# Kernel tuning notes

Measured on AMD Instinct MI355X. Metric: run time of the kernel, lower is better.

The kernel has to match this reference:

```python
import jax, jax.numpy as jnp
import numpy as np

N_NODES = 100000
N_EDGES = 3200000
D_IN = 128
D_OUT = 128

def setup_inputs() -> dict:
    key = jax.random.key(0)
    k1, k2, k3, k4, k5 = jax.random.split(key, 5)
    nodes = jnp.arange(N_NODES, dtype=jnp.int64 if jax.config.jax_enable_x64 else jnp.int32)
    features = jax.random.normal(k1, (N_NODES, D_IN), dtype=jnp.float32)
    edge_index = jax.random.randint(k2, (2, N_EDGES), 0, N_NODES)
    # torch nn.Linear(2*D_IN, D_OUT) params, stored as [in, out]
    bound = 1.0 / np.sqrt(2 * D_IN)
    W = jax.random.uniform(k3, (2 * D_IN, D_OUT), minval=-bound, maxval=bound, dtype=jnp.float32)
    b = jax.random.uniform(k4, (D_OUT,), minval=-bound, maxval=bound, dtype=jnp.float32)
    return {"nodes": nodes, "features": features, "edge_index": edge_index, "W": W, "b": b}

def reference(nodes, features, edge_index, W, b):
    # Mean aggregation over full neighbor lists. gcn=False: edges are treated
    # as undirected (neighbors appended for both src and dst), and output is
    # relu(Linear(concat([self_feats, neigh_feats]))).
    N, d = features.shape
    src, dst = edge_index[0], edge_index[1]
    neigh_sum = (jnp.zeros((N, d), features.dtype)
                 .at[src].add(features[dst])
                 .at[dst].add(features[src]))
    cnt = (jnp.zeros((N,), features.dtype)
           .at[src].add(1.0)
           .at[dst].add(1.0))
    neigh_mean = neigh_sum / jnp.maximum(cnt, 1.0)[:, None]
    combined = jnp.concatenate([features[nodes], neigh_mean[nodes]], axis=1)  # [B, 2d]
    return jax.nn.relu(combined @ W + b)
```

## Files before the change

### kernel.cpp

```cpp
#include <hip/hip_runtime.h>
#include <hip/hip_bf16.h>
#include <cmath>

#define D 128
#define MAXNB 1024
#define TEDGE 2048

typedef __attribute__((ext_vector_type(8))) short bf16x8;
typedef __attribute__((ext_vector_type(4))) float f32x4;

__device__ __forceinline__ unsigned short f2bf(float f) {
    union { __hip_bfloat16 h; unsigned short u; } c;
    c.h = __float2bfloat16(f);
    return c.u;
}

__device__ __forceinline__ void accum8(float* a, uint4 u) {
    a[0] += __uint_as_float(u.x << 16);
    a[1] += __uint_as_float(u.x & 0xffff0000u);
    a[2] += __uint_as_float(u.y << 16);
    a[3] += __uint_as_float(u.y & 0xffff0000u);
    a[4] += __uint_as_float(u.z << 16);
    a[5] += __uint_as_float(u.z & 0xffff0000u);
    a[6] += __uint_as_float(u.w << 16);
    a[7] += __uint_as_float(u.w & 0xffff0000u);
}

__device__ __forceinline__ void accum8f8(float* a, uint2 u) {
    a[0] += __builtin_amdgcn_cvt_f32_fp8((int)u.x, 0);
    a[1] += __builtin_amdgcn_cvt_f32_fp8((int)u.x, 1);
    a[2] += __builtin_amdgcn_cvt_f32_fp8((int)u.x, 2);
    a[3] += __builtin_amdgcn_cvt_f32_fp8((int)u.x, 3);
    a[4] += __builtin_amdgcn_cvt_f32_fp8((int)u.y, 0);
    a[5] += __builtin_amdgcn_cvt_f32_fp8((int)u.y, 1);
    a[6] += __builtin_amdgcn_cvt_f32_fp8((int)u.y, 2);
    a[7] += __builtin_amdgcn_cvt_f32_fp8((int)u.y, 3);
}

__global__ __launch_bounds__(256) void partition_edges(
    const int* __restrict__ ei, int* __restrict__ cursor,
    int* __restrict__ arena, int pbcap, int E, int nb) {
    __shared__ int cnt[MAXNB];
    __shared__ int off[MAXNB + 1];
    __shared__ int gb[MAXNB];
    __shared__ int sb[256];
    __shared__ int stage[2 * TEDGE];
    const int t = threadIdx.x;
    const int e0 = blockIdx.x * TEDGE;
    const int eE = min(e0 + TEDGE, E);

#pragma unroll
    for (int k = 0; k < 4; ++k) cnt[t * 4 + k] = 0;
    __syncthreads();

    int s[8], d[8];
    bool v[8];
#pragma unroll
    for (int q = 0; q < 8; ++q) {
        int e = e0 + t + q * 256;
        v[q] = e < eE;
        if (v[q]) { s[q] = ei[e]; d[q] = ei[E + e]; }
    }

#pragma unroll
    for (int q = 0; q < 8; ++q) if (v[q]) {
        atomicAdd(&cnt[s[q] >> 7], 1);
        atomicAdd(&cnt[d[q] >> 7], 1);
    }
    __syncthreads();

    int c0 = cnt[t * 4], c1 = cnt[t * 4 + 1], c2 = cnt[t * 4 + 2], c3 = cnt[t * 4 + 3];
    sb[t] = c0 + c1 + c2 + c3;
    __syncthreads();
    for (int o = 1; o < 256; o <<= 1) {
        int x = (t >= o) ? sb[t - o] : 0;
        __syncthreads();
        sb[t] += x;
        __syncthreads();
    }
    int run = (t > 0) ? sb[t - 1] : 0;
    off[t * 4] = run; run += c0;
    off[t * 4 + 1] = run; run += c1;
    off[t * 4 + 2] = run; run += c2;
    off[t * 4 + 3] = run;
    if (t == 255) off[MAXNB] = sb[255];

    for (int j = t; j < nb; j += 256) {
        int c = cnt[j];
        gb[j] = c ? atomicAdd(&cursor[j], c) : 0;
    }
    __syncthreads();

#pragma unroll
    for (int k = 0; k < 4; ++k) cnt[t * 4 + k] = off[t * 4 + k];
    __syncthreads();

#pragma unroll
    for (int q = 0; q < 8; ++q) if (v[q]) {
        int ps = atomicAdd(&cnt[s[q] >> 7], 1);
        stage[ps] = ((s[q] & 127) << 17) | d[q];
        int pd = atomicAdd(&cnt[d[q] >> 7], 1);
        stage[pd] = ((d[q] & 127) << 17) | s[q];
    }
    __syncthreads();

    const int total = 2 * (eE - e0);
    for (int p = t; p < total; p += 256) {
        int vv = stage[p];
        int lo = 0, hi = MAXNB;
        while (hi - lo > 1) {
            int mid = (lo + hi) >> 1;
            if (off[mid] <= p) lo = mid; else hi = mid;
        }
        int idx = gb[lo] + (p - off[lo]);
        if (idx < pbcap) arena[(size_t)lo * pbcap + idx] = vv;
    }
}

__global__ __launch_bounds__(256) void bucket_scatter(
    const int* __restrict__ cursor, const int* __restrict__ arena, int pbcap,
    int* __restrict__ deg, int* __restrict__ colp, int cap, int N, int nb) {
    __shared__ int ldeg[128];
    const int t = threadIdx.x;
    for (int b = blockIdx.x; b < nb; b += gridDim.x) {
        if (t < 128) ldeg[t] = 0;
        __syncthreads();
        int cnt = cursor[b];
        if (cnt > pbcap) cnt = pbcap;
        const int* s = arena + (size_t)b * pbcap;
        const size_t cb = (size_t)(b << 7) * cap;
        int i = t;
        for (; i + 768 < cnt; i += 1024) {
            int v0 = s[i], v1 = s[i + 256], v2 = s[i + 512], v3 = s[i + 768];
            int r0 = atomicAdd(&ldeg[v0 >> 17], 1);
            int r1 = atomicAdd(&ldeg[v1 >> 17], 1);
            int r2 = atomicAdd(&ldeg[v2 >> 17], 1);
            int r3 = atomicAdd(&ldeg[v3 >> 17], 1);
            if (r0 < cap) colp[cb + (size_t)(v0 >> 17) * cap + r0] = v0 & 0x1FFFF;
            if (r1 < cap) colp[cb + (size_t)(v1 >> 17) * cap + r1] = v1 & 0x1FFFF;
            if (r2 < cap) colp[cb + (size_t)(v2 >> 17) * cap + r2] = v2 & 0x1FFFF;
            if (r3 < cap) colp[cb + (size_t)(v3 >> 17) * cap + r3] = v3 & 0x1FFFF;
        }
        for (; i < cnt; i += 256) {
            int v = s[i];
            int r = atomicAdd(&ldeg[v >> 17], 1);
            if (r < cap) colp[cb + (size_t)(v >> 17) * cap + r] = v & 0x1FFFF;
        }
        __syncthreads();
        if (t < 128) {
            int node = (b << 7) + t;
            if (node < N) deg[node] = ldeg[t];
        }
        __syncthreads();
    }
}

__global__ __launch_bounds__(256) void bucket_fill(
    const int* __restrict__ ei, int* __restrict__ deg,
    int* __restrict__ colp, int cap, int E) {
    int tid = blockIdx.x * blockDim.x + threadIdx.x;
    int stride = gridDim.x * blockDim.x;
    int e[8], s[8], d[8];
    bool v[8];
#pragma unroll
    for (int q = 0; q < 8; ++q) {
        e[q] = tid + q * stride;
        v[q] = e[q] < E;
    }
#pragma unroll
    for (int q = 0; q < 8; ++q) if (v[q]) { s[q] = ei[e[q]]; d[q] = ei[E + e[q]]; }
    int rs[8], rd[8];
#pragma unroll
    for (int q = 0; q < 8; ++q) if (v[q]) rs[q] = atomicAdd(&deg[s[q]], 1);
#pragma unroll
    for (int q = 0; q < 8; ++q) if (v[q]) rd[q] = atomicAdd(&deg[d[q]], 1);
#pragma unroll
    for (int q = 0; q < 8; ++q) if (v[q] && rs[q] < cap) colp[(size_t)s[q] * cap + rs[q]] = d[q];
#pragma unroll
    for (int q = 0; q < 8; ++q) if (v[q] && rd[q] < cap) colp[(size_t)d[q] * cap + rd[q]] = s[q];
}

__global__ __launch_bounds__(256) void convert_fp8(
    const float4* __restrict__ f, uint2* __restrict__ o, int n8) {
    int i = blockIdx.x * blockDim.x + threadIdx.x;
    int stride = gridDim.x * blockDim.x;
    for (; i < n8; i += stride) {
        float4 a = f[2 * i];
        float4 c = f[2 * i + 1];
        int w0 = __builtin_amdgcn_cvt_pk_fp8_f32(a.x, a.y, 0, false);
        w0 = __builtin_amdgcn_cvt_pk_fp8_f32(a.z, a.w, w0, true);
        int w1 = __builtin_amdgcn_cvt_pk_fp8_f32(c.x, c.y, 0, false);
        w1 = __builtin_amdgcn_cvt_pk_fp8_f32(c.z, c.w, w1, true);
        uint2 r;
        r.x = (unsigned)w0;
        r.y = (unsigned)w1;
        o[i] = r;
    }
}

__global__ __launch_bounds__(256) void convert_bf16(
    const float4* __restrict__ f, uint2* __restrict__ o, int n4) {
    int i = blockIdx.x * blockDim.x + threadIdx.x;
    int stride = gridDim.x * blockDim.x;
    for (; i < n4; i += stride) {
        float4 v = f[i];
        uint2 r;
        r.x = (unsigned)f2bf(v.x) | ((unsigned)f2bf(v.y) << 16);
        r.y = (unsigned)f2bf(v.z) | ((unsigned)f2bf(v.w) << 16);
        o[i] = r;
    }
}

__global__ __launch_bounds__(256) void prepack_w(
    const float* __restrict__ W, unsigned* __restrict__ wb) {
    int id = blockIdx.x * 256 + threadIdx.x;
    if (id >= 4096) return;
    int j = id & 127, ks = id >> 7;
    unsigned hi[4], lo[4];
#pragma unroll
    for (int e = 0; e < 4; ++e) {
        float w0 = W[(size_t)(ks * 8 + 2 * e) * 128 + j];
        float w1 = W[(size_t)(ks * 8 + 2 * e + 1) * 128 + j];
        unsigned short h0 = f2bf(w0), h1 = f2bf(w1);
        float l0f = w0 - __uint_as_float((unsigned)h0 << 16);
        float l1f = w1 - __uint_as_float((unsigned)h1 << 16);
        hi[e] = (unsigned)h0 | ((unsigned)h1 << 16);
        lo[e] = (unsigned)f2bf(l0f) | ((unsigned)f2bf(l1f) << 16);
    }
    ((uint4*)wb)[ks * 128 + j] = make_uint4(hi[0], hi[1], hi[2], hi[3]);
    ((uint4*)wb)[4096 + ks * 128 + j] = make_uint4(lo[0], lo[1], lo[2], lo[3]);
}

__global__ __launch_bounds__(256) void gather_gemm_pad(
    const int* __restrict__ nodes, const float* __restrict__ feat,
    const uint2* __restrict__ fb2,
    const int* __restrict__ deg, const int* __restrict__ colp, int cap,
    const uint4* __restrict__ wb4, const float* __restrict__ b,
    float* __restrict__ out, int B) {
    __shared__ uint4 combQ[512];
    unsigned char* combB = (unsigned char*)combQ;
    const int t = threadIdx.x;
    const int lane = t & 63;
    const int w = t >> 6;
    const int g = lane >> 4;
    const int sub = lane & 15;
    const int base = blockIdx.x * 16;

    {
        int r = t >> 4, sb = t & 15;
        int row = base + r;
        uint4 u = make_uint4(0u, 0u, 0u, 0u);
        if (row < B) {
            const float* fp = feat + (size_t)nodes[row] * D + sb * 8;
            float4 a = *(const float4*)fp;
            float4 c = *(const float4*)(fp + 4);
            u.x = (unsigned)f2bf(a.x) | ((unsigned)f2bf(a.y) << 16);
            u.y = (unsigned)f2bf(a.z) | ((unsigned)f2bf(a.w) << 16);
            u.z = (unsigned)f2bf(c.x) | ((unsigned)f2bf(c.y) << 16);
            u.w = (unsigned)f2bf(c.z) | ((unsigned)f2bf(c.w) << 16);
        }
        int off = (r * 512 + sb * 16) ^ ((r & 7) << 4);
        *(uint4*)(combB + off) = u;
    }

    for (int rq = 0; rq < 4; ++rq) {
        const int rl = w + 4 * rq;
        const int row = base + rl;
        if (row < B) {
            const int node = __builtin_amdgcn_readfirstlane(nodes[row]);
            int degn = deg[node];
            if (degn > cap) degn = cap;
            const int p0 = node * cap;
            float accA[8] = {0, 0, 0, 0, 0, 0, 0, 0};
            float accB[8] = {0, 0, 0, 0, 0, 0, 0, 0};
            int i = 0;
            for (; i + 15 < degn; i += 16) {
                int n0 = colp[p0 + i + g];
                int n1 = colp[p0 + i + 4 + g];
                int n2 = colp[p0 + i + 8 + g];
                int n3 = colp[p0 + i + 12 + g];
                uint2 u0 = fb2[(size_t)n0 * 16 + sub];
                uint2 u1 = fb2[(size_t)n1 * 16 + sub];
                uint2 u2 = fb2[(size_t)n2 * 16 + sub];
                uint2 u3 = fb2[(size_t)n3 * 16 + sub];
                accum8f8(accA, u0);
                accum8f8(accB, u1);
                accum8f8(accA, u2);
                accum8f8(accB, u3);
            }
            for (; i + 7 < degn; i += 8) {
                int n0 = colp[p0 + i + g];
                int n1 = colp[p0 + i + 4 + g];
                uint2 u0 = fb2[(size_t)n0 * 16 + sub];
                uint2 u1 = fb2[(size_t)n1 * 16 + sub];
                accum8f8(accA, u0);
                accum8f8(accB, u1);
            }
            for (; i + 3 < degn; i += 4) {
                int n0 = colp[p0 + i + g];
                accum8f8(accA, fb2[(size_t)n0 * 16 + sub]);
            }
            int rem = degn - i;
            if (g < rem) {
                int n0 = colp[p0 + i + g];
                accum8f8(accB, fb2[(size_t)n0 * 16 + sub]);
            }
            const float inv = (degn > 0) ? 1.0f / (float)degn : 0.0f;
            float vals[8];
#pragma unroll
            for (int k = 0; k < 8; ++k) {
                float v = accA[k] + accB[k];
                v += __shfl_xor(v, 16, 64);
                v += __shfl_xor(v, 32, 64);
                vals[k] = v * inv;
            }
            if (g == 0) {
                unsigned p0u = (unsigned)f2bf(vals[0]) | ((unsigned)f2bf(vals[1]) << 16);
                unsigned p1u = (unsigned)f2bf(vals[2]) | ((unsigned)f2bf(vals[3]) << 16);
                unsigned p2u = (unsigned)f2bf(vals[4]) | ((unsigned)f2bf(vals[5]) << 16);
                unsigned p3u = (unsigned)f2bf(vals[6]) | ((unsigned)f2bf(vals[7]) << 16);
                int off = (rl * 512 + 256 + sub * 16) ^ ((rl & 7) << 4);
                *(uint4*)(combB + off) = make_uint4(p0u, p1u, p2u, p3u);
            }
        } else if (g == 0) {
            int off = (rl * 512 + 256 + sub * 16) ^ ((rl & 7) << 4);
            *(uint4*)(combB + off) = make_uint4(0u, 0u, 0u, 0u);
        }
    }
    __syncthreads();

    const int jl = lane & 15;
    const int kg = lane >> 4;
    const int j0 = w * 32 + jl, j1 = j0 + 16;
    f32x4 acc0 = {0.f, 0.f, 0.f, 0.f};
    f32x4 acc1 = {0.f, 0.f, 0.f, 0.f};
#pragma unroll
    for (int s = 0; s < 8; ++s) {
        int aoff = (jl * 512 + s * 64 + kg * 16) ^ ((jl & 7) << 4);
        bf16x8 a = *(const bf16x8*)(combB + aoff);
        int bi = (s * 4 + kg) * 128;
        bf16x8 bh0 = *(const bf16x8*)&wb4[bi + j0];
        bf16x8 bh1 = *(const bf16x8*)&wb4[bi + j1];
        bf16x8 bl0 = *(const bf16x8*)&wb4[4096 + bi + j0];
        bf16x8 bl1 = *(const bf16x8*)&wb4[4096 + bi + j1];
        acc0 = __builtin_amdgcn_mfma_f32_16x16x32_bf16(a, bh0, acc0, 0, 0, 0);
        acc1 = __builtin_amdgcn_mfma_f32_16x16x32_bf16(a, bh1, acc1, 0, 0, 0);
        acc0 = __builtin_amdgcn_mfma_f32_16x16x32_bf16(a, bl0, acc0, 0, 0, 0);
        acc1 = __builtin_amdgcn_mfma_f32_16x16x32_bf16(a, bl1, acc1, 0, 0, 0);
    }
    const float b0 = b[j0], b1 = b[j1];
    const int r0 = kg * 4;
#pragma unroll
    for (int rg = 0; rg < 4; ++rg) {
        int row = base + r0 + rg;
        if (row < B) {
            out[(size_t)row * D + j0] = fmaxf(acc0[rg] + b0, 0.0f);
            out[(size_t)row * D + j1] = fmaxf(acc1[rg] + b1, 0.0f);
        }
    }
}


__global__ __launch_bounds__(256) void deg_rank(
    const int* __restrict__ ei, int* __restrict__ deg,
    unsigned* __restrict__ rank, int E) {
    int tid = blockIdx.x * blockDim.x + threadIdx.x;
    int stride = gridDim.x * blockDim.x;
    int e[8], s[8], d[8];
    bool v[8];
#pragma unroll
    for (int q = 0; q < 8; ++q) {
        e[q] = tid + q * stride;
        v[q] = e[q] < E;
    }
#pragma unroll
    for (int q = 0; q < 8; ++q) if (v[q]) { s[q] = ei[e[q]]; d[q] = ei[E + e[q]]; }
    int rs[8], rd[8];
#pragma unroll
    for (int q = 0; q < 8; ++q) if (v[q]) rs[q] = atomicAdd(&deg[s[q]], 1);
#pragma unroll
    for (int q = 0; q < 8; ++q) if (v[q]) rd[q] = atomicAdd(&deg[d[q]], 1);
#pragma unroll
    for (int q = 0; q < 8; ++q)
        if (v[q]) rank[e[q]] = (unsigned)rs[q] | ((unsigned)rd[q] << 16);
}

__global__ __launch_bounds__(256) void scan_block(
    const int* __restrict__ deg, int* __restrict__ rowptr,
    int* __restrict__ bsum, int N) {
    __shared__ int lds[256];
    const int t = threadIdx.x;
    const int base = blockIdx.x * 1024 + t * 4;
    int v[4];
#pragma unroll
    for (int k = 0; k < 4; ++k) v[k] = (base + k < N) ? deg[base + k] : 0;
    lds[t] = v[0] + v[1] + v[2] + v[3];
    __syncthreads();
    for (int off = 1; off < 256; off <<= 1) {
        int x = (t >= off) ? lds[t - off] : 0;
        __syncthreads();
        lds[t] += x;
        __syncthreads();
    }
    if (t == 255) bsum[blockIdx.x] = lds[255];
    int run = (t > 0) ? lds[t - 1] : 0;
#pragma unroll
    for (int k = 0; k < 4; ++k) {
        if (base + k < N) rowptr[base + k] = run;
        run += v[k];
    }
}

__global__ __launch_bounds__(1024) void scan_aux(int* __restrict__ bsum, int nb) {
    __shared__ int lds[1024];
    const int t = threadIdx.x;
    int v = (t < nb) ? bsum[t] : 0;
    lds[t] = v;
    __syncthreads();
    for (int off = 1; off < 1024; off <<= 1) {
        int x = (t >= off) ? lds[t - off] : 0;
        __syncthreads();
        lds[t] += x;
        __syncthreads();
    }
    if (t < nb) bsum[t] = lds[t] - v;
}

__global__ __launch_bounds__(256) void scan_finalize(
    int* __restrict__ rowptr, const int* __restrict__ bsum, int N, int twoE) {
    int i = blockIdx.x * blockDim.x + threadIdx.x;
    if (i == 0) rowptr[N] = twoE;
    if (i >= N) return;
    rowptr[i] += bsum[i >> 10];
}

__global__ __launch_bounds__(256) void csr_fill2(
    const int* __restrict__ ei, const int* __restrict__ rowptr,
    const unsigned* __restrict__ rank, int* __restrict__ col, int E) {
    int tid = blockIdx.x * blockDim.x + threadIdx.x;
    int stride = gridDim.x * blockDim.x;
    int e[8], s[8], d[8], ps[8], pd[8];
    unsigned r[8];
    bool v[8];
#pragma unroll
    for (int q = 0; q < 8; ++q) {
        e[q] = tid + q * stride;
        v[q] = e[q] < E;
    }
#pragma unroll
    for (int q = 0; q < 8; ++q) if (v[q]) { s[q] = ei[e[q]]; d[q] = ei[E + e[q]]; r[q] = rank[e[q]]; }
#pragma unroll
    for (int q = 0; q < 8; ++q) if (v[q]) { ps[q] = rowptr[s[q]]; pd[q] = rowptr[d[q]]; }
#pragma unroll
    for (int q = 0; q < 8; ++q) if (v[q]) {
        col[ps[q] + (int)(r[q] & 0xffffu)] = d[q];
        col[pd[q] + (int)(r[q] >> 16)] = s[q];
    }
}

__global__ __launch_bounds__(256) void gather_gemm(
    const int* __restrict__ nodes, const uint4* __restrict__ fb4,
    const int* __restrict__ rowptr, const int* __restrict__ col,
    const float* __restrict__ W, const float* __restrict__ b,
    float* __restrict__ out, int B) {
    __shared__ float comb[16][256];
    const int t = threadIdx.x;
    const int lane = t & 63;
    const int w = t >> 6;
    const int g = lane >> 4;
    const int sub = lane & 15;
    const int base = blockIdx.x * 16;
    {
        int r = t >> 4, sb = t & 15;
        int row = base + r;
        float a[8] = {0, 0, 0, 0, 0, 0, 0, 0};
        if (row < B) accum8(a, fb4[(size_t)nodes[row] * 16 + sb]);
        *(float4*)&comb[r][sb * 8] = make_float4(a[0], a[1], a[2], a[3]);
        *(float4*)&comb[r][sb * 8 + 4] = make_float4(a[4], a[5], a[6], a[7]);
    }
    for (int rq = 0; rq < 4; ++rq) {
        const int rl = w + 4 * rq;
        const int row = base + rl;
        if (row < B) {
            const int node = __builtin_amdgcn_readfirstlane(nodes[row]);
            const int p0 = rowptr[node], p1 = rowptr[node + 1];
            float accA[8] = {0, 0, 0, 0, 0, 0, 0, 0};
            float accB[8] = {0, 0, 0, 0, 0, 0, 0, 0};
            int i = p0;
            for (; i + 7 < p1; i += 8) {
                int na = col[i + g];
                int nb = col[i + 4 + g];
                uint4 ua = fb4[(size_t)na * 16 + sub];
                uint4 ub = fb4[(size_t)nb * 16 + sub];
                accum8(accA, ua);
                accum8(accB, ub);
            }
            for (; i + 3 < p1; i += 4) {
                int na = col[i + g];
                accum8(accA, fb4[(size_t)na * 16 + sub]);
            }
            int rem = p1 - i;
            if (g < rem) {
                int na = col[i + g];
                accum8(accB, fb4[(size_t)na * 16 + sub]);
            }
            const int degn = p1 - p0;
            const float inv = (degn > 0) ? 1.0f / (float)degn : 0.0f;
            float vals[8];
#pragma unroll
            for (int k = 0; k < 8; ++k) {
                float v = accA[k] + accB[k];
                v += __shfl_xor(v, 16, 64);
                v += __shfl_xor(v, 32, 64);
                vals[k] = v * inv;
            }
            if (g == 0) {
                *(float4*)&comb[rl][128 + sub * 8] =
                    make_float4(vals[0], vals[1], vals[2], vals[3]);
                *(float4*)&comb[rl][128 + sub * 8 + 4] =
                    make_float4(vals[4], vals[5], vals[6], vals[7]);
            }
        } else if (g == 0) {
            float4 z = make_float4(0.f, 0.f, 0.f, 0.f);
            *(float4*)&comb[rl][128 + sub * 8] = z;
            *(float4*)&comb[rl][128 + sub * 8 + 4] = z;
        }
    }
    __syncthreads();
    const int j = t & 127;
    const int rr = t >> 7;
    float acc[8];
    const float bj = b[j];
#pragma unroll
    for (int r = 0; r < 8; ++r) acc[r] = bj;
    for (int k4 = 0; k4 < 64; ++k4) {
        float w0 = W[(size_t)(4 * k4 + 0) * 128 + j];
        float w1 = W[(size_t)(4 * k4 + 1) * 128 + j];
        float w2 = W[(size_t)(4 * k4 + 2) * 128 + j];
        float w3 = W[(size_t)(4 * k4 + 3) * 128 + j];
#pragma unroll
        for (int r = 0; r < 8; ++r) {
            float4 c = *(const float4*)&comb[2 * r + rr][4 * k4];
            acc[r] = fmaf(c.x, w0, acc[r]);
            acc[r] = fmaf(c.y, w1, acc[r]);
            acc[r] = fmaf(c.z, w2, acc[r]);
            acc[r] = fmaf(c.w, w3, acc[r]);
        }
    }
#pragma unroll
    for (int r = 0; r < 8; ++r) {
        int row = base + 2 * r + rr;
        if (row < B) out[(size_t)row * D + j] = fmaxf(acc[r], 0.0f);
    }
}

__global__ __launch_bounds__(256) void edge_scatter(
    const int* __restrict__ ei, const float* __restrict__ feat,
    float* __restrict__ nsum, float* __restrict__ cnt, int E) {
    long long tid = (long long)blockIdx.x * blockDim.x + threadIdx.x;
    int e = (int)(tid >> 7);
    if (e >= E) return;
    int d = (int)(tid & 127);
    int src = ei[e];
    int dst = ei[E + e];
    atomicAdd(&nsum[(size_t)src * D + d], feat[(size_t)dst * D + d]);
    atomicAdd(&nsum[(size_t)dst * D + d], feat[(size_t)src * D + d]);
    if (d == 0) {
        atomicAdd(&cnt[src], 1.0f);
        atomicAdd(&cnt[dst], 1.0f);
    }
}

__global__ __launch_bounds__(256) void sage_out(
    const int* __restrict__ nodes, const float* __restrict__ feat,
    const float* nsum, const float* __restrict__ cnt,
    const float* __restrict__ W, const float* __restrict__ b,
    float* out, int B) {
    __shared__ float comb[16][256];
    const int t = threadIdx.x;
    const int j = t & 127;
    const int rr = t >> 7;
    const int base = blockIdx.x * 16;
    for (int r = 0; r < 16; ++r) {
        int row = base + r;
        float v = 0.0f;
        if (row < B) {
            int node = nodes[row];
            if (t < 128) v = feat[(size_t)node * D + t];
            else v = nsum[(size_t)node * D + (t - 128)] / fmaxf(cnt[node], 1.0f);
        }
        comb[r][t] = v;
    }
    __syncthreads();
    float acc[8];
    const float bj = b[j];
#pragma unroll
    for (int r = 0; r < 8; ++r) acc[r] = bj;
#pragma unroll 4
    for (int k = 0; k < 256; ++k) {
        float wj = W[(size_t)k * 128 + j];
#pragma unroll
        for (int r = 0; r < 8; ++r) acc[r] += comb[rr + 2 * r][k] * wj;
    }
#pragma unroll
    for (int r = 0; r < 8; ++r) {
        int row = base + rr + 2 * r;
        if (row < B) out[(size_t)row * D + j] = fmaxf(acc[r], 0.0f);
    }
}

extern "C" void kernel_launch(void* const* d_in, const int* in_sizes, int n_in,
                              void* d_out, int out_size, void* d_ws, size_t ws_size,
                              hipStream_t stream) {
    const int* nodes = (const int*)d_in[0];
    const float* feat = (const float*)d_in[1];
    const int* ei = (const int*)d_in[2];
    const float* W = (const float*)d_in[3];
    const float* b = (const float*)d_in[4];
    float* out = (float*)d_out;

    const int B = in_sizes[0];
    const int N = in_sizes[1] / D;
    const int E = in_sizes[2] / 2;
    const int twoE = 2 * E;
    const int nscan = (N + 1023) / 1024;
    const int n4 = N * (D / 4);
    const int n8 = N * (D / 8);
    const size_t ws_ints = ws_size / sizeof(int);

    const int nb = (N + 127) >> 7;
    double avgpb = nb > 0 ? (2.0 * (double)E) / (double)nb : 0.0;
    int pbcap = (int)(avgpb + 8.0 * sqrt(avgpb > 0.0 ? avgpb : 0.0) + 64.0);
    pbcap = (pbcap + 3) & ~3;
    const size_t u_arena = (size_t)nb * pbcap;
    const size_t u_fp8 = (size_t)N * 32;
    const size_t u0 = (u_arena > u_fp8) ? u_arena : u_fp8;
    const size_t o0_deg = (u0 + 3) & ~(size_t)3;
    const size_t o0_cur = (o0_deg + N + 3) & ~(size_t)3;
    const size_t o0_wb = o0_cur + 1024;
    const size_t o0_colp = o0_wb + 32768;
    long long cap0_ll = (ws_ints > o0_colp) ? (long long)((ws_ints - o0_colp) / N) : 0;
    int cap0 = (cap0_ll > 192) ? 192 : (int)cap0_ll;

    const size_t o1_deg = (size_t)N * 32;
    const size_t o1_wb = (o1_deg + N + 3) & ~(size_t)3;
    const size_t o1_colp = o1_wb + 32768;
    long long cap_ll = (ws_ints > o1_colp) ? (long long)((ws_ints - o1_colp) / N) : 0;
    int cap = (cap_ll > 192) ? 192 : (int)cap_ll;

    const size_t o_deg = 0;
    const size_t o_rowptr = (o_deg + N + 3) & ~(size_t)3;
    const size_t o_bsum = (o_rowptr + N + 1 + 3) & ~(size_t)3;
    const size_t o_col = (o_bsum + 1024 + 3) & ~(size_t)3;
    const size_t o_rank = (o_col + twoE + 3) & ~(size_t)3;
    const size_t tail = ((size_t)E > (size_t)N * 64) ? (size_t)E : (size_t)N * 64;
    const size_t need2 = (o_rank + tail) * sizeof(int);

    if (cap0 >= 128 && N <= (1 << 17) && nb <= MAXNB && E > 0) {
        int* wsI = (int*)d_ws;
        int* arena = wsI;
        unsigned* f8 = (unsigned*)wsI;
        int* deg = wsI + o0_deg;
        int* cursor = wsI + o0_cur;
        unsigned* wbp = (unsigned*)(wsI + o0_wb);
        int* colp = wsI + o0_colp;

        hipMemsetAsync(cursor, 0, 1024 * sizeof(int), stream);

        prepack_w<<<16, 256, 0, stream>>>(W, wbp);

        int pblocks = (E + TEDGE - 1) / TEDGE;
        partition_edges<<<pblocks, 256, 0, stream>>>(ei, cursor, arena, pbcap, E, nb);

        bucket_scatter<<<nb, 256, 0, stream>>>(
            cursor, arena, pbcap, deg, colp, cap0, N, nb);

        convert_fp8<<<(n8 + 1023) / 1024, 256, 0, stream>>>(
            (const float4*)feat, (uint2*)f8, n8);

        gather_gemm_pad<<<(B + 15) / 16, 256, 0, stream>>>(
            nodes, feat, (const uint2*)f8, deg, colp, cap0,
            (const uint4*)wbp, b, out, B);
    } else if (cap >= 128) {
        int* wsI = (int*)d_ws;
        unsigned* f8 = (unsigned*)wsI;
        int* deg = wsI + o1_deg;
        unsigned* wbp = (unsigned*)(wsI + o1_wb);
        int* colp = wsI + o1_colp;

        hipMemsetAsync(deg, 0, (size_t)N * sizeof(int), stream);

        prepack_w<<<16, 256, 0, stream>>>(W, wbp);

        convert_fp8<<<(n8 + 1023) / 1024, 256, 0, stream>>>(
            (const float4*)feat, (uint2*)f8, n8);

        int eb8 = (E + 2047) / 2048;
        bucket_fill<<<eb8, 256, 0, stream>>>(ei, deg, colp, cap, E);

        gather_gemm_pad<<<(B + 15) / 16, 256, 0, stream>>>(
            nodes, feat, (const uint2*)f8, deg, colp, cap,
            (const uint4*)wbp, b, out, B);
    } else if (ws_size >= need2 && nscan <= 1024) {
        int* wsI = (int*)d_ws;
        int* deg = wsI + o_deg;
        int* rowptr = wsI + o_rowptr;
        int* bsum = wsI + o_bsum;
        int* col = wsI + o_col;
        unsigned* rank = (unsigned*)(wsI + o_rank);
        unsigned* fbu = (unsigned*)(wsI + o_rank);

        hipMemsetAsync(deg, 0, (size_t)N * sizeof(int), stream);

        int eb8 = (E + 2047) / 2048;
        deg_rank<<<eb8, 256, 0, stream>>>(ei, deg, rank, E);
        scan_block<<<nscan, 256, 0, stream>>>(deg, rowptr, bsum, N);
        scan_aux<<<1, 1024, 0, stream>>>(bsum, nscan);
        scan_finalize<<<(N + 255) / 256, 256, 0, stream>>>(rowptr, bsum, N, twoE);
        csr_fill2<<<eb8, 256, 0, stream>>>(ei, rowptr, rank, col, E);
        convert_bf16<<<(n4 + 1023) / 1024, 256, 0, stream>>>(
            (const float4*)feat, (uint2*)fbu, n4);
        gather_gemm<<<(B + 15) / 16, 256, 0, stream>>>(
            nodes, (const uint4*)fbu, rowptr, col, W, b, out, B);
    } else {
        float* nsum = out;
        float* cnt = (float*)d_ws;
        hipMemsetAsync(d_out, 0, (size_t)N * D * sizeof(float), stream);
        hipMemsetAsync(d_ws, 0, (size_t)N * sizeof(float), stream);
        long long tot = (long long)E * 128;
        int blocks = (int)((tot + 255) / 256);
        edge_scatter<<<blocks, 256, 0, stream>>>(ei, feat, nsum, cnt, E);
        sage_out<<<(B + 15) / 16, 256, 0, stream>>>(nodes, feat, nsum, cnt, W, b, out, B);
    }
}
```

Before: 389.9 us.

## Pad bucket cursors, record bucket ids in staging, unroll gather, use packed fp8 convert

Pads the per-bucket global cursor array so each atomic counter sits on its own 64-byte line, which cuts false-sharing contention between blocks. In partition_edges, the bucket id of each staged edge is kept in a shared ushort array, replacing the per-element binary search over the offsets. The gather loop gets an extra 32-wide unrolled tier for more outstanding loads, and the fp8 decode uses packed two-value conversions. Costs are extra shared memory, a larger memset, and higher register pressure in the gather kernel.

```diff
diff --git a/kernel.cpp b/kernel.cpp
--- a/kernel.cpp
+++ b/kernel.cpp
@@ -5,9 +5,11 @@
 #define D 128
 #define MAXNB 1024
 #define TEDGE 2048
+#define CURPAD 16
 
 typedef __attribute__((ext_vector_type(8))) short bf16x8;
 typedef __attribute__((ext_vector_type(4))) float f32x4;
+typedef __attribute__((ext_vector_type(2))) float f32x2;
 
 __device__ __forceinline__ unsigned short f2bf(float f) {
     union { __hip_bfloat16 h; unsigned short u; } c;
@@ -27,14 +29,12 @@
 }
 
 __device__ __forceinline__ void accum8f8(float* a, uint2 u) {
-    a[0] += __builtin_amdgcn_cvt_f32_fp8((int)u.x, 0);
-    a[1] += __builtin_amdgcn_cvt_f32_fp8((int)u.x, 1);
-    a[2] += __builtin_amdgcn_cvt_f32_fp8((int)u.x, 2);
-    a[3] += __builtin_amdgcn_cvt_f32_fp8((int)u.x, 3);
-    a[4] += __builtin_amdgcn_cvt_f32_fp8((int)u.y, 0);
-    a[5] += __builtin_amdgcn_cvt_f32_fp8((int)u.y, 1);
-    a[6] += __builtin_amdgcn_cvt_f32_fp8((int)u.y, 2);
-    a[7] += __builtin_amdgcn_cvt_f32_fp8((int)u.y, 3);
+    f32x2 p0 = __builtin_amdgcn_cvt_pk_f32_fp8((int)u.x, false);
+    f32x2 p1 = __builtin_amdgcn_cvt_pk_f32_fp8((int)u.x, true);
+    f32x2 p2 = __builtin_amdgcn_cvt_pk_f32_fp8((int)u.y, false);
+    f32x2 p3 = __builtin_amdgcn_cvt_pk_f32_fp8((int)u.y, true);
+    a[0] += p0.x; a[1] += p0.y; a[2] += p1.x; a[3] += p1.y;
+    a[4] += p2.x; a[5] += p2.y; a[6] += p3.x; a[7] += p3.y;
 }
 
 __global__ __launch_bounds__(256) void partition_edges(
@@ -45,6 +45,7 @@
     __shared__ int gb[MAXNB];
     __shared__ int sb[256];
     __shared__ int stage[2 * TEDGE];
+    __shared__ unsigned short stageb[2 * TEDGE];
     const int t = threadIdx.x;
     const int e0 = blockIdx.x * TEDGE;
     const int eE = min(e0 + TEDGE, E);
@@ -87,7 +88,7 @@
 
     for (int j = t; j < nb; j += 256) {
         int c = cnt[j];
-        gb[j] = c ? atomicAdd(&cursor[j], c) : 0;
+        gb[j] = c ? atomicAdd(&cursor[j * CURPAD], c) : 0;
     }
     __syncthreads();
 
@@ -97,23 +98,22 @@
 
 #pragma unroll
     for (int q = 0; q < 8; ++q) if (v[q]) {
-        int ps = atomicAdd(&cnt[s[q] >> 7], 1);
+        int bs = s[q] >> 7, bd = d[q] >> 7;
+        int ps = atomicAdd(&cnt[bs], 1);
         stage[ps] = ((s[q] & 127) << 17) | d[q];
-        int pd = atomicAdd(&cnt[d[q] >> 7], 1);
+        stageb[ps] = (unsigned short)bs;
+        int pd = atomicAdd(&cnt[bd], 1);
         stage[pd] = ((d[q] & 127) << 17) | s[q];
+        stageb[pd] = (unsigned short)bd;
     }
     __syncthreads();
 
     const int total = 2 * (eE - e0);
     for (int p = t; p < total; p += 256) {
         int vv = stage[p];
-        int lo = 0, hi = MAXNB;
-        while (hi - lo > 1) {
-            int mid = (lo + hi) >> 1;
-            if (off[mid] <= p) lo = mid; else hi = mid;
-        }
-        int idx = gb[lo] + (p - off[lo]);
-        if (idx < pbcap) arena[(size_t)lo * pbcap + idx] = vv;
+        int bkt = stageb[p];
+        int idx = gb[bkt] + (p - off[bkt]);
+        if (idx < pbcap) arena[(size_t)bkt * pbcap + idx] = vv;
     }
 }
 
@@ -125,7 +125,7 @@
     for (int b = blockIdx.x; b < nb; b += gridDim.x) {
         if (t < 128) ldeg[t] = 0;
         __syncthreads();
-        int cnt = cursor[b];
+        int cnt = cursor[b * CURPAD];
         if (cnt > pbcap) cnt = pbcap;
         const int* s = arena + (size_t)b * pbcap;
         const size_t cb = (size_t)(b << 7) * cap;
@@ -274,6 +274,32 @@
             float accA[8] = {0, 0, 0, 0, 0, 0, 0, 0};
             float accB[8] = {0, 0, 0, 0, 0, 0, 0, 0};
             int i = 0;
+            for (; i + 31 < degn; i += 32) {
+                int n0 = colp[p0 + i + g];
+                int n1 = colp[p0 + i + 4 + g];
+                int n2 = colp[p0 + i + 8 + g];
+                int n3 = colp[p0 + i + 12 + g];
+                int n4 = colp[p0 + i + 16 + g];
+                int n5 = colp[p0 + i + 20 + g];
+                int n6 = colp[p0 + i + 24 + g];
+                int n7 = colp[p0 + i + 28 + g];
+                uint2 u0 = fb2[(size_t)n0 * 16 + sub];
+                uint2 u1 = fb2[(size_t)n1 * 16 + sub];
+                uint2 u2 = fb2[(size_t)n2 * 16 + sub];
+                uint2 u3 = fb2[(size_t)n3 * 16 + sub];
+                uint2 u4 = fb2[(size_t)n4 * 16 + sub];
+                uint2 u5 = fb2[(size_t)n5 * 16 + sub];
+                uint2 u6 = fb2[(size_t)n6 * 16 + sub];
+                uint2 u7 = fb2[(size_t)n7 * 16 + sub];
+                accum8f8(accA, u0);
+                accum8f8(accB, u1);
+                accum8f8(accA, u2);
+                accum8f8(accB, u3);
+                accum8f8(accA, u4);
+                accum8f8(accB, u5);
+                accum8f8(accA, u6);
+                accum8f8(accB, u7);
+            }
             for (; i + 15 < degn; i += 16) {
                 int n0 = colp[p0 + i + g];
                 int n1 = colp[p0 + i + 4 + g];
@@ -637,7 +663,7 @@
     const size_t u0 = (u_arena > u_fp8) ? u_arena : u_fp8;
     const size_t o0_deg = (u0 + 3) & ~(size_t)3;
     const size_t o0_cur = (o0_deg + N + 3) & ~(size_t)3;
-    const size_t o0_wb = o0_cur + 1024;
+    const size_t o0_wb = o0_cur + 1024 * CURPAD;
     const size_t o0_colp = o0_wb + 32768;
     long long cap0_ll = (ws_ints > o0_colp) ? (long long)((ws_ints - o0_colp) / N) : 0;
     int cap0 = (cap0_ll > 192) ? 192 : (int)cap0_ll;
@@ -665,7 +691,7 @@
         unsigned* wbp = (unsigned*)(wsI + o0_wb);
         int* colp = wsI + o0_colp;
 
-        hipMemsetAsync(cursor, 0, 1024 * sizeof(int), stream);
+        hipMemsetAsync(cursor, 0, 1024 * CURPAD * sizeof(int), stream);
 
         prepack_w<<<16, 256, 0, stream>>>(W, wbp);
 
```

New measurement: 413.4 us. 1.06x slower.
